# Kernel tuning notes

Hardware: AMD Instinct MI355X
Metric: run time of the kernel (lower is better)

Reference implementation:

```python
import jax, jax.numpy as jnp
import numpy as np

B, IN_F, OUT_F, KD = 256, 1024, 128, 16


def setup_inputs() -> dict:
    key = jax.random.key(0)
    k1, k2 = jax.random.split(key)
    x = jax.random.normal(k1, (B, IN_F), dtype=jnp.float32)
    t_mat = jax.random.normal(k2, (IN_F, OUT_F, KD), dtype=jnp.float32)
    return {"x": x, "t_mat": t_mat}


def reference(x, t_mat):
    # Projection: [B, in] @ [in, out*kd] -> [B, out, kd]
    m = jnp.einsum('bi,iok->bok', x, t_mat)
    # All-pairs L1 distance over kernel dim: [B, B, out]
    norm = jnp.sum(jnp.abs(m[:, None, :, :] - m[None, :, :, :]), axis=-1)
    # exp(-norm) summed over the partner axis; subtract 1 for self-pair (norm=0 -> exp=1)
    o_b = jnp.sum(jnp.exp(-norm), axis=1) - 1.0  # [B, out]
    return jnp.concatenate([x, o_b], axis=1)  # [B, in + out]
```

## Files before the change

### kernel.cpp

```cpp
#include <hip/hip_runtime.h>
#include <hip/hip_fp16.h>


#define BATCH 256
#define INF   1024
#define OUTF  128
#define KDIM  16
#define TCOLS 2048
#define OCOLS 1152
#define XB    1032

typedef __attribute__((ext_vector_type(8))) short short8;
typedef __attribute__((ext_vector_type(4))) float f32x4;

__device__ inline unsigned pack_bf2(float lo, float hi) {
    return __builtin_amdgcn_perm(__float_as_uint(hi), __float_as_uint(lo), 0x07060302u);
}
__device__ inline unsigned short bf_trunc(float f) {
    return (unsigned short)(__float_as_uint(f) >> 16);
}

__global__ __launch_bounds__(256, 2) void k_gemm(const float* __restrict__ x,
                                                 const float* __restrict__ T,
                                                 __half* __restrict__ mh) {
    const int blk = blockIdx.x;
    const int o   = blk & 127;
    const int mq  = blk >> 7;
    const int tid = threadIdx.x;
    const int wave = tid >> 6, lane = tid & 63;
    const int l15 = lane & 15, q = lane >> 4;

    __shared__ unsigned short bs[16][XB];
    __shared__ __half pmout[64][16];

    {
        const int kb = tid >> 2, n0 = (tid & 3) * 4;
        #pragma unroll
        for (int pass = 0; pass < 16; ++pass) {
            const int k = pass * 64 + kb;
            float4 v = *reinterpret_cast<const float4*>(&T[k * TCOLS + o * KDIM + n0]);
            bs[n0 + 0][k] = bf_trunc(v.x);
            bs[n0 + 1][k] = bf_trunc(v.y);
            bs[n0 + 2][k] = bf_trunc(v.z);
            bs[n0 + 3][k] = bf_trunc(v.w);
        }
    }
    __syncthreads();

    const int mt = mq * 4 + wave;
    const float* xr = &x[(mt * 16 + l15) * INF + q * 8];

    float4 st[4][2];
    #pragma unroll
    for (int p = 0; p < 4; ++p) {
        st[p][0] = *reinterpret_cast<const float4*>(xr + p * 32);
        st[p][1] = *reinterpret_cast<const float4*>(xr + p * 32 + 4);
    }
    f32x4 acc = {0.f, 0.f, 0.f, 0.f};
    #pragma unroll
    for (int ks = 0; ks < 32; ++ks) {
        const int p = ks & 3;
        float4 a0 = st[p][0], a1 = st[p][1];
        const int kn = (ks + 4 < 32) ? ks + 4 : ks;
        st[p][0] = *reinterpret_cast<const float4*>(xr + kn * 32);
        st[p][1] = *reinterpret_cast<const float4*>(xr + kn * 32 + 4);
        short8 bfr = *reinterpret_cast<const short8*>(&bs[l15][ks * 32 + q * 8]);
        union { unsigned u[4]; short8 s; } ua;
        ua.u[0] = pack_bf2(a0.x, a0.y); ua.u[1] = pack_bf2(a0.z, a0.w);
        ua.u[2] = pack_bf2(a1.x, a1.y); ua.u[3] = pack_bf2(a1.z, a1.w);
        acc = __builtin_amdgcn_mfma_f32_16x16x32_bf16(ua.s, bfr, acc, 0, 0, 0);
    }

    #pragma unroll
    for (int r = 0; r < 4; ++r)
        pmout[wave * 16 + q * 4 + r][l15] = __float2half(acc[r]);
    __syncthreads();

    if (tid < 128) {
        const int row = tid >> 1, hh = tid & 1;
        uint4 v = *reinterpret_cast<const uint4*>(&pmout[row][hh * 8]);
        *reinterpret_cast<uint4*>(&mh[o * (BATCH * KDIM) + (mq * 64 + row) * KDIM + hh * 8]) = v;
    }
}

__global__ __launch_bounds__(1024) void k_pair(const float* __restrict__ x,
                                               const __half* __restrict__ mh,
                                               float* __restrict__ out) {
    const int blk = blockIdx.x;
    const int o   = blk & 127;
    const int h   = blk >> 7;
    const int tid = threadIdx.x;

    __shared__ __half2 pm[BATCH][8];
    __shared__ float part[32][128];

    if (tid < 256)
        reinterpret_cast<float4*>(out)[blk * 288 + tid] =
            reinterpret_cast<const float4*>(x)[blk * 256 + tid];

    if (tid < 512) {
        uint4 v = *reinterpret_cast<const uint4*>(
            &mh[o * (BATCH * KDIM) + (tid >> 1) * KDIM + (tid & 1) * 8]);
        *reinterpret_cast<uint4*>(&pm[tid >> 1][(tid & 1) * 4]) = v;
    }
    __syncthreads();

    const int i1 = tid & 31;
    const int bsel = tid >> 5;
    __half2 my[4][8];
    #pragma unroll
    for (int r = 0; r < 4; ++r) {
        union { uint4 u[2]; __half2 hh[8]; } c;
        c.u[0] = *reinterpret_cast<const uint4*>(&pm[h * 128 + r * 32 + i1][0]);
        c.u[1] = *reinterpret_cast<const uint4*>(&pm[h * 128 + r * 32 + i1][4]);
        #pragma unroll
        for (int j = 0; j < 8; ++j) my[r][j] = c.hh[j];
    }

    float tot[4] = {0.f, 0.f, 0.f, 0.f};
    const int b2_lo = bsel * 8;
    #pragma unroll
    for (int b2 = b2_lo; b2 < b2_lo + 8; ++b2) {
        union { uint4 u[2]; __half2 hh[8]; } co;
        co.u[0] = *reinterpret_cast<const uint4*>(&pm[b2][0]);
        co.u[1] = *reinterpret_cast<const uint4*>(&pm[b2][4]);
        #pragma unroll
        for (int r = 0; r < 4; ++r) {
            __half2 e0 = __habs2(__hsub2(my[r][0], co.hh[0]));
            __half2 e1 = __habs2(__hsub2(my[r][1], co.hh[1]));
            __half2 e2 = __habs2(__hsub2(my[r][2], co.hh[2]));
            __half2 e3 = __habs2(__hsub2(my[r][3], co.hh[3]));
            e0 = __hadd2(e0, __habs2(__hsub2(my[r][4], co.hh[4])));
            e1 = __hadd2(e1, __habs2(__hsub2(my[r][5], co.hh[5])));
            e2 = __hadd2(e2, __habs2(__hsub2(my[r][6], co.hh[6])));
            e3 = __hadd2(e3, __habs2(__hsub2(my[r][7], co.hh[7])));
            __half2 es = __hadd2(__hadd2(e0, e1), __hadd2(e2, e3));
            float n = __low2float(es) + __high2float(es);
            tot[r] += __expf(-n);
        }
    }
    #pragma unroll
    for (int r = 0; r < 4; ++r)
        part[bsel][r * 32 + i1] = tot[r];
    __syncthreads();

    if (tid < 128) {
        float s = -1.0f;
        #pragma unroll
        for (int j = 0; j < 32; ++j) s += part[j][tid];
        out[(h * 128 + tid) * OCOLS + INF + o] = s;
    }
}

extern "C" void kernel_launch(void* const* d_in, const int* in_sizes, int n_in,
                              void* d_out, int out_size, void* d_ws, size_t ws_size,
                              hipStream_t stream) {
    const float* x = (const float*)d_in[0];
    const float* T = (const float*)d_in[1];
    float* out = (float*)d_out;
    __half* mh = (__half*)d_ws;

    k_gemm<<<512, 256, 0, stream>>>(x, T, mh);
    k_pair<<<256, 1024, 0, stream>>>(x, mh, out);
}
```

Baseline: 88.38 us.

## Fuse projection GEMM and pairwise L1-exp kernel into one launch

Merges the bf16 MFMA projection kernel and the pairwise distance kernel into a single 1024-thread kernel. Each block computes the full 256-row projection for its output feature directly into shared memory, removing the workspace round-trip and a second launch. In exchange, the GEMM and T loads are duplicated across the two batch-half blocks per feature, and fewer, larger blocks run.

```diff
diff --git a/kernel.cpp b/kernel.cpp
--- a/kernel.cpp
+++ b/kernel.cpp
@@ -20,24 +20,29 @@
     return (unsigned short)(__float_as_uint(f) >> 16);
 }
 
-__global__ __launch_bounds__(256, 2) void k_gemm(const float* __restrict__ x,
-                                                 const float* __restrict__ T,
-                                                 __half* __restrict__ mh) {
+__global__ __launch_bounds__(1024, 1) void k_fused(const float* __restrict__ x,
+                                                   const float* __restrict__ T,
+                                                   float* __restrict__ out) {
     const int blk = blockIdx.x;
     const int o   = blk & 127;
-    const int mq  = blk >> 7;
+    const int h   = blk >> 7;
     const int tid = threadIdx.x;
     const int wave = tid >> 6, lane = tid & 63;
     const int l15 = lane & 15, q = lane >> 4;
 
     __shared__ unsigned short bs[16][XB];
-    __shared__ __half pmout[64][16];
+    __shared__ __half2 pm[BATCH][8];
+    __shared__ float part[32][128];
+
+    if (tid < 256)
+        reinterpret_cast<float4*>(out)[blk * 288 + tid] =
+            reinterpret_cast<const float4*>(x)[blk * 256 + tid];
 
     {
         const int kb = tid >> 2, n0 = (tid & 3) * 4;
         #pragma unroll
-        for (int pass = 0; pass < 16; ++pass) {
-            const int k = pass * 64 + kb;
+        for (int pass = 0; pass < 4; ++pass) {
+            const int k = pass * 256 + kb;
             float4 v = *reinterpret_cast<const float4*>(&T[k * TCOLS + o * KDIM + n0]);
             bs[n0 + 0][k] = bf_trunc(v.x);
             bs[n0 + 1][k] = bf_trunc(v.y);
@@ -47,8 +52,7 @@
     }
     __syncthreads();
 
-    const int mt = mq * 4 + wave;
-    const float* xr = &x[(mt * 16 + l15) * INF + q * 8];
+    const float* xr = &x[(wave * 16 + l15) * INF + q * 8];
 
     float4 st[4][2];
     #pragma unroll
@@ -71,37 +75,11 @@
         acc = __builtin_amdgcn_mfma_f32_16x16x32_bf16(ua.s, bfr, acc, 0, 0, 0);
     }
 
-    #pragma unroll
-    for (int r = 0; r < 4; ++r)
-        pmout[wave * 16 + q * 4 + r][l15] = __float2half(acc[r]);
-    __syncthreads();
-
-    if (tid < 128) {
-        const int row = tid >> 1, hh = tid & 1;
-        uint4 v = *reinterpret_cast<const uint4*>(&pmout[row][hh * 8]);
-        *reinterpret_cast<uint4*>(&mh[o * (BATCH * KDIM) + (mq * 64 + row) * KDIM + hh * 8]) = v;
-    }
-}
-
-__global__ __launch_bounds__(1024) void k_pair(const float* __restrict__ x,
-                                               const __half* __restrict__ mh,
-                                               float* __restrict__ out) {
-    const int blk = blockIdx.x;
-    const int o   = blk & 127;
-    const int h   = blk >> 7;
-    const int tid = threadIdx.x;
-
-    __shared__ __half2 pm[BATCH][8];
-    __shared__ float part[32][128];
-
-    if (tid < 256)
-        reinterpret_cast<float4*>(out)[blk * 288 + tid] =
-            reinterpret_cast<const float4*>(x)[blk * 256 + tid];
-
-    if (tid < 512) {
-        uint4 v = *reinterpret_cast<const uint4*>(
-            &mh[o * (BATCH * KDIM) + (tid >> 1) * KDIM + (tid & 1) * 8]);
-        *reinterpret_cast<uint4*>(&pm[tid >> 1][(tid & 1) * 4]) = v;
+    {
+        __half* pmh = reinterpret_cast<__half*>(pm);
+        #pragma unroll
+        for (int r = 0; r < 4; ++r)
+            pmh[(wave * 16 + q * 4 + r) * 16 + l15] = __float2half(acc[r]);
     }
     __syncthreads();
 
@@ -158,8 +136,7 @@
     const float* x = (const float*)d_in[0];
     const float* T = (const float*)d_in[1];
     float* out = (float*)d_out;
-    __half* mh = (__half*)d_ws;
+    (void)d_ws; (void)ws_size;
 
-    k_gemm<<<512, 256, 0, stream>>>(x, T, mh);
-    k_pair<<<256, 1024, 0, stream>>>(x, mh, out);
+    k_fused<<<256, 1024, 0, stream>>>(x, T, out);
 }
```

New measurement: 98.85 us. 11.8% more time.
